# Kernel optimization log

Measured on AMD Instinct MI355X. Metric: run time of the kernel, lower is better.

Reference implementation:

```python
import jax, jax.numpy as jnp
import numpy as np

B, J, D = 524288, 17, 3
THRESHOLD = 2.0  # __init__ arg; module stores half_body = threshold / 2
HALF_BODY = THRESHOLD / 2.0


def setup_inputs() -> dict:
    key = jax.random.key(0)
    kps_world_pred = jax.random.normal(key, (B, J, D), dtype=jnp.float32)
    return {"kps_world_pred": kps_world_pred}


def reference(kps_world_pred) -> jnp.ndarray:
    # per-(batch, joint) L2 norm of the 3D world coordinate
    dist = jnp.linalg.norm(kps_world_pred, axis=-1)  # [B, J]
    # threshold-gated accumulation: only norms > half_body contribute
    loss = jnp.where(dist > HALF_BODY, dist, 0.0).sum()
    normalization = kps_world_pred.shape[0] * kps_world_pred.shape[1]
    return loss / normalization
```

## Files before the change

kernel.cpp:

```cpp
#include <hip/hip_runtime.h>


#define GRID1 2048
#define BLOCK 256
#define CHUNK_F4 768

__global__ __launch_bounds__(BLOCK) void body_loss_partial(
    const float4* __restrict__ p4, float* __restrict__ partial, int nchunks) {
    __shared__ float4 lds[CHUNK_F4];
    const int t = threadIdx.x;
    float acc = 0.0f;

    for (int c = blockIdx.x; c < nchunks; c += GRID1) {
        const int base = c * CHUNK_F4;
        const float4 g0 = p4[base + t];
        const float4 g1 = p4[base + 256 + t];
        const float4 g2 = p4[base + 512 + t];
        __syncthreads();
        lds[t]       = g0;
        lds[256 + t] = g1;
        lds[512 + t] = g2;
        __syncthreads();
        const float4 v0 = lds[3 * t + 0];
        const float4 v1 = lds[3 * t + 1];
        const float4 v2 = lds[3 * t + 2];
        const float d0 = sqrtf(v0.x * v0.x + v0.y * v0.y + v0.z * v0.z);
        const float d1 = sqrtf(v0.w * v0.w + v1.x * v1.x + v1.y * v1.y);
        const float d2 = sqrtf(v1.z * v1.z + v1.w * v1.w + v2.x * v2.x);
        const float d3 = sqrtf(v2.y * v2.y + v2.z * v2.z + v2.w * v2.w);
        acc += (d0 > 1.0f ? d0 : 0.0f);
        acc += (d1 > 1.0f ? d1 : 0.0f);
        acc += (d2 > 1.0f ? d2 : 0.0f);
        acc += (d3 > 1.0f ? d3 : 0.0f);
    }

    #pragma unroll
    for (int off = 32; off > 0; off >>= 1)
        acc += __shfl_down(acc, off, 64);

    __shared__ float wsum[4];
    const int lane = t & 63, wid = t >> 6;
    if (lane == 0) wsum[wid] = acc;
    __syncthreads();
    if (t == 0)
        partial[blockIdx.x] = wsum[0] + wsum[1] + wsum[2] + wsum[3];
}

__global__ __launch_bounds__(BLOCK) void body_loss_final(
    const float* __restrict__ partial, float* __restrict__ out, float inv_norm) {
    const int t = threadIdx.x;
    float acc = 0.0f;
    #pragma unroll
    for (int k = 0; k < GRID1 / BLOCK; ++k)
        acc += partial[k * BLOCK + t];
    #pragma unroll
    for (int off = 32; off > 0; off >>= 1)
        acc += __shfl_down(acc, off, 64);
    __shared__ float wsum[4];
    const int lane = t & 63, wid = t >> 6;
    if (lane == 0) wsum[wid] = acc;
    __syncthreads();
    if (t == 0)
        out[0] = (wsum[0] + wsum[1] + wsum[2] + wsum[3]) * inv_norm;
}

extern "C" void kernel_launch(void* const* d_in, const int* in_sizes, int n_in,
                              void* d_out, int out_size, void* d_ws, size_t ws_size,
                              hipStream_t stream) {
    const float* in = (const float*)d_in[0];
    float* out = (float*)d_out;
    float* partial = (float*)d_ws;

    const long long nfloats  = in_sizes[0];
    const long long ntriples = nfloats / 3;
    const int nchunks = (int)(nfloats / (CHUNK_F4 * 4));
    const float inv_norm = 1.0f / (float)ntriples;

    body_loss_partial<<<GRID1, BLOCK, 0, stream>>>(
        (const float4*)in, partial, nchunks);
    body_loss_final<<<1, BLOCK, 0, stream>>>(partial, out, inv_norm);
}
```

Baseline: 23.54 us.

## Double-buffer LDS staging and prefetch next chunk with nontemporal loads

Restructures the grid-stride loop so that the global loads for the next chunk are issued before the current chunk is processed out of a second LDS buffer. This drops one barrier per iteration and overlaps memory latency with the compute. Global loads also become nontemporal to avoid polluting the caches on a streaming read. The first chunk is loaded without checking whether it exists, so a launch with fewer chunks than blocks would read past the end of the input. The second LDS buffer doubles shared memory use per block.

```diff
diff --git a/kernel.cpp b/kernel.cpp
--- a/kernel.cpp
+++ b/kernel.cpp
@@ -3,35 +3,51 @@
 
 #define GRID1 2048
 #define BLOCK 256
-#define CHUNK_F4 768
+#define CF4   768
+
+typedef float vf4 __attribute__((ext_vector_type(4)));
 
 __global__ __launch_bounds__(BLOCK) void body_loss_partial(
-    const float4* __restrict__ p4, float* __restrict__ partial, int nchunks) {
-    __shared__ float4 lds[CHUNK_F4];
+    const vf4* __restrict__ p4, float* __restrict__ partial, int nchunks) {
+    __shared__ vf4 lds[2][CF4];
     const int t = threadIdx.x;
     float acc = 0.0f;
 
-    for (int c = blockIdx.x; c < nchunks; c += GRID1) {
-        const int base = c * CHUNK_F4;
-        const float4 g0 = p4[base + t];
-        const float4 g1 = p4[base + 256 + t];
-        const float4 g2 = p4[base + 512 + t];
-        __syncthreads();
-        lds[t]       = g0;
-        lds[256 + t] = g1;
-        lds[512 + t] = g2;
-        __syncthreads();
-        const float4 v0 = lds[3 * t + 0];
-        const float4 v1 = lds[3 * t + 1];
-        const float4 v2 = lds[3 * t + 2];
-        const float d0 = sqrtf(v0.x * v0.x + v0.y * v0.y + v0.z * v0.z);
-        const float d1 = sqrtf(v0.w * v0.w + v1.x * v1.x + v1.y * v1.y);
-        const float d2 = sqrtf(v1.z * v1.z + v1.w * v1.w + v2.x * v2.x);
-        const float d3 = sqrtf(v2.y * v2.y + v2.z * v2.z + v2.w * v2.w);
-        acc += (d0 > 1.0f ? d0 : 0.0f);
-        acc += (d1 > 1.0f ? d1 : 0.0f);
-        acc += (d2 > 1.0f ? d2 : 0.0f);
-        acc += (d3 > 1.0f ? d3 : 0.0f);
+    int c = blockIdx.x;
+    {
+        const vf4* g = p4 + (size_t)c * CF4;
+        vf4 r0 = __builtin_nontemporal_load(&g[t]);
+        vf4 r1 = __builtin_nontemporal_load(&g[256 + t]);
+        vf4 r2 = __builtin_nontemporal_load(&g[512 + t]);
+        int cur = 0;
+        lds[0][t] = r0; lds[0][256 + t] = r1; lds[0][512 + t] = r2;
+
+        int next = c + GRID1;
+        while (true) {
+            const bool have_next = next < nchunks;
+            if (have_next) {
+                const vf4* gn = p4 + (size_t)next * CF4;
+                r0 = __builtin_nontemporal_load(&gn[t]);
+                r1 = __builtin_nontemporal_load(&gn[256 + t]);
+                r2 = __builtin_nontemporal_load(&gn[512 + t]);
+            }
+            __syncthreads();
+            const vf4 v0 = lds[cur][3 * t + 0];
+            const vf4 v1 = lds[cur][3 * t + 1];
+            const vf4 v2 = lds[cur][3 * t + 2];
+            const float d0 = sqrtf(v0.x * v0.x + v0.y * v0.y + v0.z * v0.z);
+            const float d1 = sqrtf(v0.w * v0.w + v1.x * v1.x + v1.y * v1.y);
+            const float d2 = sqrtf(v1.z * v1.z + v1.w * v1.w + v2.x * v2.x);
+            const float d3 = sqrtf(v2.y * v2.y + v2.z * v2.z + v2.w * v2.w);
+            acc += (d0 > 1.0f ? d0 : 0.0f);
+            acc += (d1 > 1.0f ? d1 : 0.0f);
+            acc += (d2 > 1.0f ? d2 : 0.0f);
+            acc += (d3 > 1.0f ? d3 : 0.0f);
+            if (!have_next) break;
+            cur ^= 1;
+            lds[cur][t] = r0; lds[cur][256 + t] = r1; lds[cur][512 + t] = r2;
+            next += GRID1;
+        }
     }
 
     #pragma unroll
@@ -73,10 +89,10 @@
 
     const long long nfloats  = in_sizes[0];
     const long long ntriples = nfloats / 3;
-    const int nchunks = (int)(nfloats / (CHUNK_F4 * 4));
+    const int nchunks = (int)(nfloats / (CF4 * 4));
     const float inv_norm = 1.0f / (float)ntriples;
 
     body_loss_partial<<<GRID1, BLOCK, 0, stream>>>(
-        (const float4*)in, partial, nchunks);
+        (const vf4*)in, partial, nchunks);
     body_loss_final<<<1, BLOCK, 0, stream>>>(partial, out, inv_norm);
 }
```

Result: faster. 21.04 us (-10.6%).
